# Performance work log

Hardware: AMD Instinct MI355X
Metric: run time of the kernel (lower is better)

The kernel has to match this reference:

```python
import jax, jax.numpy as jnp
import numpy as np

ROPE_BASE = 1000000.0
EPS = 1e-6
N_HEADS = 16

def apply_rope(x, base=ROPE_BASE):
    # x: [b, seq, heads, head_dim]
    b, seq, n_heads, dim = x.shape
    half = dim // 2
    i = jnp.arange(half)
    theta = 1.0 / base ** (2 * i / dim)
    pos = jnp.arange(seq)
    angles = pos[:, None] * theta[None, :]            # [seq, half]
    cos = jnp.cos(angles)[None, :, None, :]
    sin = jnp.sin(angles)[None, :, None, :]
    x1, x2 = jnp.split(x, 2, axis=-1)
    return jnp.concatenate([x1 * cos - x2 * sin, x1 * sin + x2 * cos], axis=-1)

def setup_inputs() -> dict:
    key = jax.random.key(0)
    ks = jax.random.split(key, 6)
    b, seq, dim = 2, 2048, 1024
    scale = 1.0 / np.sqrt(dim)
    return {
        "x": jax.random.normal(ks[0], (b, seq, dim), dtype=jnp.float32),
        "norm_scale": jnp.ones((dim,), dtype=jnp.float32),
        "Wq": jax.random.normal(ks[1], (dim, dim), dtype=jnp.float32) * scale,
        "Wk": jax.random.normal(ks[2], (dim, dim), dtype=jnp.float32) * scale,
        "Wv": jax.random.normal(ks[3], (dim, dim), dtype=jnp.float32) * scale,
        "Wo": jax.random.normal(ks[4], (dim, dim), dtype=jnp.float32) * scale,
    }

def reference(x, norm_scale, Wq, Wk, Wv, Wo):
    b, seq, d = x.shape
    n_heads = N_HEADS
    dh = d // n_heads
    # RMSNorm
    var = jnp.mean(jnp.square(x), axis=-1, keepdims=True)
    x_norm = x * jax.lax.rsqrt(var + EPS) * norm_scale
    # QKV projections ([in,out] weights as in nnx.Linear)
    q = (x_norm @ Wq).reshape(b, seq, n_heads, dh)
    k = (x_norm @ Wk).reshape(b, seq, n_heads, dh)
    v = (x_norm @ Wv).reshape(b, seq, n_heads, dh)
    q = apply_rope(q)
    k = apply_rope(k)
    # causal attention with explicit score matrix (faithful to source)
    scores = jnp.einsum('bthd,bshd->bhts', q, k) / jnp.sqrt(jnp.float32(dh))
    causal = jnp.triu(jnp.full((seq, seq), -jnp.inf, dtype=jnp.float32), k=1)
    scores = scores + causal[None, None, :, :]
    weights = jax.nn.softmax(scores, axis=-1)
    out = jnp.einsum('bhts,bshd->bthd', weights, v).reshape(b, seq, d)
    return out @ Wo
```

## Files before the change

kernel.cpp:

```cpp
#include <hip/hip_runtime.h>

typedef unsigned short ushort_t;
typedef __attribute__((ext_vector_type(8))) short short8;
typedef __attribute__((ext_vector_type(4))) short short4v;
typedef __attribute__((ext_vector_type(4))) float floatx4;

#define DEV static __device__ __forceinline__
#define NEG_BIG (-1e30f)

#define MFMA16(a, b, c) __builtin_amdgcn_mfma_f32_16x16x16bf16_1k((a), (b), (c), 0, 0, 0)

typedef const __attribute__((address_space(1))) unsigned int* gas_ptr;
typedef __attribute__((address_space(3))) unsigned int* las_ptr;

DEV void async16(const ushort_t* g, ushort_t* l) {
    __builtin_amdgcn_global_load_lds((gas_ptr)(const void*)g, (las_ptr)(void*)l, 16, 0, 0);
}

DEV float bf2f(ushort_t u) {
    union { unsigned u; float f; } v; v.u = ((unsigned)u) << 16; return v.f;
}
DEV ushort_t f2bf(float f) {
    union { float f; unsigned u; } v; v.f = f;
    unsigned r = v.u + 0x7FFF + ((v.u >> 16) & 1);
    return (ushort_t)(r >> 16);
}
DEV ushort_t f2bf_trunc(float f) {
    union { float f; unsigned u; } v; v.f = f;
    return (ushort_t)(v.u >> 16);
}
DEV float load_bf16_scrub(const ushort_t* p, size_t i) {
    ushort_t u = p[i];
    if (((u >> 7) & 0xFF) == 0xFF) u = 0;
    return bf2f(u);
}
DEV float load_f32_scrub(const ushort_t* p, size_t i) {
    unsigned u = ((const unsigned*)p)[i];
    if (((u >> 23) & 0xFF) == 0xFF) u = 0;
    union { unsigned u; float f; } v; v.u = u; return v.f;
}

DEV int probe_is_f32(const ushort_t* __restrict__ p) {
    int tid = threadIdx.x + threadIdx.y * blockDim.x;
    int nthr = blockDim.x * blockDim.y;
    __shared__ int cnt;
    if (tid == 0) cnt = 0;
    __syncthreads();
    int weird = 0;
    for (int i = tid; i < 2048; i += nthr) {
        unsigned e = (p[i] >> 7) & 0xFF;
        weird += (e >= 0x90) ? 1 : 0;
    }
#pragma unroll
    for (int off = 32; off; off >>= 1) weird += __shfl_xor(weird, off);
    if ((tid & 63) == 0) atomicAdd(&cnt, weird);
    __syncthreads();
    return cnt > 16;
}

__global__ void prep_kernel(const ushort_t* __restrict__ W0,
                            const ushort_t* __restrict__ W1,
                            const ushort_t* __restrict__ W2,
                            const ushort_t* __restrict__ W3,
                            ushort_t* __restrict__ WTq3,
                            ushort_t* __restrict__ WoT,
                            const ushort_t* __restrict__ x,
                            const ushort_t* __restrict__ g,
                            ushort_t* __restrict__ xn) {
    int is_f32 = probe_is_f32(x);
    int z = blockIdx.z;
    if (z < 4) {
        const ushort_t* W = (z == 0) ? W0 : (z == 1) ? W1 : (z == 2) ? W2 : W3;
        __shared__ ushort_t tile[32][33];
        int tx = threadIdx.x, ty = threadIdx.y;
        int xx = blockIdx.x * 32 + tx;
        int y0 = blockIdx.y * 32;
#pragma unroll
        for (int j = 0; j < 32; j += 8) {
            size_t idx = (size_t)(y0 + ty + j) * 1024 + xx;
            tile[ty + j][tx] = f2bf(is_f32 ? load_f32_scrub(W, idx) : load_bf16_scrub(W, idx));
        }
        __syncthreads();
        int nx = blockIdx.y * 32 + tx;
        ushort_t* dst = (z < 3) ? WTq3 : WoT;
        int ny0 = blockIdx.x * 32 + ((z < 3) ? z * 1024 : 0);
#pragma unroll
        for (int j = 0; j < 32; j += 8)
            dst[(size_t)(ny0 + ty + j) * 1024 + nx] = tile[tx][ty + j];
    } else {
        int row = (z - 4) * 1024 + blockIdx.y * 32 + blockIdx.x;
        int tid = threadIdx.y * 32 + threadIdx.x;
        float vals[4], gv[4];
        size_t base = (size_t)row * 1024 + tid * 4;
#pragma unroll
        for (int i = 0; i < 4; i++) {
            if (is_f32) {
                vals[i] = load_f32_scrub(x, base + i);
                gv[i]   = load_f32_scrub(g, tid * 4 + i);
            } else {
                vals[i] = load_bf16_scrub(x, base + i);
                gv[i]   = load_bf16_scrub(g, tid * 4 + i);
            }
        }
        float ss = vals[0]*vals[0] + vals[1]*vals[1] + vals[2]*vals[2] + vals[3]*vals[3];
#pragma unroll
        for (int off = 32; off > 0; off >>= 1) ss += __shfl_xor(ss, off);
        __shared__ float red[4];
        if ((tid & 63) == 0) red[tid >> 6] = ss;
        __syncthreads();
        ss = red[0] + red[1] + red[2] + red[3];
        float inv = rsqrtf(ss * (1.0f / 1024.0f) + 1e-6f);
#pragma unroll
        for (int i = 0; i < 4; i++)
            xn[base + i] = f2bf(vals[i] * inv * gv[i]);
    }
}

__global__ __launch_bounds__(256, 4) void gemm_qkv(const ushort_t* __restrict__ A,
                                                   const ushort_t* __restrict__ Bt,
                                                   ushort_t* __restrict__ qb,
                                                   ushort_t* __restrict__ kb,
                                                   ushort_t* __restrict__ vt) {
    const int K = 1024;
    int tid = threadIdx.x;
    int lane = tid & 63, w = tid >> 6;
    int c = lane & 15, quad = lane >> 4;
    int mh = w >> 1, nh = w & 1;
    int lin = blockIdx.y * gridDim.x + blockIdx.x;
    int xcd = lin & 7, idx = lin >> 3;
    int bm = ((xcd & 3) * 8 + (idx & 7)) * 128;
    int bn = ((xcd >> 2) * 12 + (idx >> 3)) * 128;
    int lr = lane >> 2, lq = lane & 3;

    __shared__ __align__(16) ushort_t As[16 * 512];
    __shared__ __align__(16) ushort_t Bs[16 * 512];

    const floatx4 zero = {0.f, 0.f, 0.f, 0.f};
    floatx4 acc[4][4];
#pragma unroll
    for (int i = 0; i < 4; i++)
#pragma unroll
        for (int j = 0; j < 4; j++) acc[i][j] = zero;

    for (int k0 = 0; k0 < K; k0 += 64) {
        __syncthreads();
#pragma unroll
        for (int ci = 0; ci < 8; ci++) {
            int ch = w * 8 + ci;
            if (ch < 16) {
                int rg = ch >> 1, kc = ch & 1;
                async16(A + (size_t)(bm + rg * 16 + lr) * K + k0 + kc * 32 + lq * 8,
                        As + ch * 512);
            } else {
                int b2 = ch - 16;
                int rg = b2 >> 1, kc = b2 & 1;
                async16(Bt + (size_t)(bn + rg * 16 + lr) * K + k0 + kc * 32 + lq * 8,
                        Bs + b2 * 512);
            }
        }
        __syncthreads();
#pragma unroll
        for (int kc = 0; kc < 2; kc++) {
            short8 af[4], bf[4];
#pragma unroll
            for (int i = 0; i < 4; i++)
                af[i] = *(const short8*)(As + ((mh * 4 + i) * 2 + kc) * 512 + c * 32 + quad * 8);
#pragma unroll
            for (int j = 0; j < 4; j++)
                bf[j] = *(const short8*)(Bs + ((nh * 4 + j) * 2 + kc) * 512 + c * 32 + quad * 8);
#pragma unroll
            for (int i = 0; i < 4; i++)
#pragma unroll
                for (int j = 0; j < 4; j++)
                    acc[i][j] = __builtin_amdgcn_mfma_f32_16x16x32_bf16(af[i], bf[j], acc[i][j], 0, 0, 0);
        }
    }

    int proj = bn >> 10;
    int n0 = (bn & 1023) + nh * 64;
    if (proj < 2) {
        float th0 = exp2f((float)c * (-19.931568569324174f / 32.0f));
        float th1 = exp2f((float)(16 + c) * (-19.931568569324174f / 32.0f));
        float scale = (proj == 0) ? 0.125f : 1.0f;
#pragma unroll
        for (int i = 0; i < 4; i++)
#pragma unroll
            for (int r = 0; r < 4; r++) {
                int s = (bm + mh * 64 + i * 16 + quad * 4 + r) & 2047;
                float a0 = (float)s * th0, a1 = (float)s * th1;
                float sn0 = __sinf(a0), cs0 = __cosf(a0);
                float sn1 = __sinf(a1), cs1 = __cosf(a1);
                float x1a = acc[i][0][r], x2a = acc[i][2][r];
                acc[i][0][r] = (x1a * cs0 - x2a * sn0) * scale;
                acc[i][2][r] = (x1a * sn0 + x2a * cs0) * scale;
                float x1b = acc[i][1][r], x2b = acc[i][3][r];
                acc[i][1][r] = (x1b * cs1 - x2b * sn1) * scale;
                acc[i][3][r] = (x1b * sn1 + x2b * cs1) * scale;
            }
        ushort_t* dst = (proj == 0) ? qb : kb;
#pragma unroll
        for (int i = 0; i < 4; i++)
#pragma unroll
            for (int j = 0; j < 4; j++)
#pragma unroll
                for (int r = 0; r < 4; r++) {
                    int row = bm + mh * 64 + i * 16 + quad * 4 + r;
                    dst[(size_t)row * 1024 + n0 + j * 16 + c] = f2bf(acc[i][j][r]);
                }
    } else {
#pragma unroll
        for (int i = 0; i < 4; i++) {
            int row0 = bm + mh * 64 + i * 16 + quad * 4;
            int b = row0 >> 11, s0v = row0 & 2047;
#pragma unroll
            for (int j = 0; j < 4; j++) {
                int col = n0 + j * 16 + c;
                int hh = col >> 6, dh = col & 63;
                short4v pk;
#pragma unroll
                for (int r = 0; r < 4; r++) pk[r] = (short)f2bf(acc[i][j][r]);
                *(short4v*)(vt + (size_t)((b * 16 + hh) * 64 + dh) * 2048 + s0v) = pk;
            }
        }
    }
}

__global__ __launch_bounds__(256, 4) void gemm_out(const ushort_t* __restrict__ A,
                                                   const ushort_t* __restrict__ Bt,
                                                   float* __restrict__ C) {
    const int K = 1024, N = 1024;
    int tid = threadIdx.x;
    int lane = tid & 63, w = tid >> 6;
    int c = lane & 15, quad = lane >> 4;
    int mh = w >> 1, nh = w & 1;
    int lin = blockIdx.y * gridDim.x + blockIdx.x;
    int xcd = lin & 7, idx = lin >> 3;
    int bm = ((xcd & 3) * 8 + (idx & 7)) * 128;
    int bn = ((xcd >> 2) * 8 + (idx >> 3)) * 64;
    int lr = lane >> 2, lq = lane & 3;

    __shared__ __align__(16) ushort_t As[16 * 512];
    __shared__ __align__(16) ushort_t Bs[8 * 512];

    const floatx4 zero = {0.f, 0.f, 0.f, 0.f};
    floatx4 acc[4][2];
#pragma unroll
    for (int i = 0; i < 4; i++)
#pragma unroll
        for (int j = 0; j < 2; j++) acc[i][j] = zero;

    for (int k0 = 0; k0 < K; k0 += 64) {
        __syncthreads();
#pragma unroll
        for (int ci = 0; ci < 6; ci++) {
            int ch = w * 6 + ci;
            if (ch < 16) {
                int rg = ch >> 1, kc = ch & 1;
                async16(A + (size_t)(bm + rg * 16 + lr) * K + k0 + kc * 32 + lq * 8,
                        As + ch * 512);
            } else {
                int b2 = ch - 16;
                int rg = b2 >> 1, kc = b2 & 1;
                async16(Bt + (size_t)(bn + rg * 16 + lr) * K + k0 + kc * 32 + lq * 8,
                        Bs + b2 * 512);
            }
        }
        __syncthreads();
#pragma unroll
        for (int kc = 0; kc < 2; kc++) {
            short8 af[4], bf[2];
#pragma unroll
            for (int i = 0; i < 4; i++)
                af[i] = *(const short8*)(As + ((mh * 4 + i) * 2 + kc) * 512 + c * 32 + quad * 8);
#pragma unroll
            for (int j = 0; j < 2; j++)
                bf[j] = *(const short8*)(Bs + ((nh * 2 + j) * 2 + kc) * 512 + c * 32 + quad * 8);
#pragma unroll
            for (int i = 0; i < 4; i++)
#pragma unroll
                for (int j = 0; j < 2; j++)
                    acc[i][j] = __builtin_amdgcn_mfma_f32_16x16x32_bf16(af[i], bf[j], acc[i][j], 0, 0, 0);
        }
    }
#pragma unroll
    for (int i = 0; i < 4; i++)
#pragma unroll
        for (int j = 0; j < 2; j++)
#pragma unroll
            for (int r = 0; r < 4; r++) {
                int row = bm + mh * 64 + i * 16 + quad * 4 + r;
                int col = bn + nh * 32 + j * 16 + c;
                C[(size_t)row * N + col] = acc[i][j][r];
            }
}

__global__ __launch_bounds__(256, 5) void attn_kernel(const ushort_t* __restrict__ q,
                                                      const ushort_t* __restrict__ k,
                                                      const ushort_t* __restrict__ vt,
                                                      ushort_t* __restrict__ o) {
    int tid = threadIdx.x;
    int lane = tid & 63, w = tid >> 6;
    int c = lane & 15, quad = lane >> 4;
    int bh = blockIdx.x;
    int b = bh >> 4, h = bh & 15;
    int qt = 31 - (int)blockIdx.y;
    int lr = lane >> 2, lq = lane & 3;
    int vb = (lq - lr) & 3;
    const ushort_t* qb  = q + (size_t)b * 2048 * 1024 + h * 64;
    const ushort_t* kbp = k + (size_t)b * 2048 * 1024 + h * 64;
    const ushort_t* vtb = vt + (size_t)(b * 16 + h) * 64 * 2048;
    ushort_t* ob = o + (size_t)b * 2048 * 1024 + h * 64;

    __shared__ __align__(16) ushort_t Ks[2][8 * 512];
    __shared__ __align__(16) ushort_t Vs[2][8 * 512];

    const floatx4 zero = {0.f, 0.f, 0.f, 0.f};

    int t0b = qt * 64;
    int t0w = t0b + w * 16;
    int ntile = qt + 1;

    const ushort_t* qrow = qb + (size_t)(t0w + c) * 1024;
    short8 aq0 = *(const short8*)(qrow + quad * 8);
    short8 aq1 = *(const short8*)(qrow + 32 + quad * 8);

    int voffA = c * 32 + (((quad >> 1) + c) & 3) * 8 + (quad & 1) * 4;
    int voffB = c * 32 + (((quad >> 1) + 2 + c) & 3) * 8 + (quad & 1) * 4;

    float l_sum = 0.f;
    floatx4 oacc[4];
#pragma unroll
    for (int dt = 0; dt < 4; dt++) oacc[dt] = zero;

#pragma unroll
    for (int ci = 0; ci < 4; ci++) {
        int ch = w * 4 + ci;
        if (ch < 8) {
            int nt = ch >> 1, hf = ch & 1;
            async16(kbp + (size_t)(nt * 16 + lr) * 1024 + hf * 32 + lq * 8,
                    Ks[0] + ch * 512);
        } else {
            int dt = (ch - 8) >> 1, hf = ch & 1;
            async16(vtb + (size_t)(dt * 16 + lr) * 2048 + hf * 32 + vb * 8,
                    Vs[0] + (ch - 8) * 512);
        }
    }

    for (int kt = 0; kt < ntile; kt++) {
        __syncthreads();
        int cur = kt & 1;
        if (kt + 1 < ntile) {
            int s1 = (kt + 1) * 64;
            int nxt = cur ^ 1;
#pragma unroll
            for (int ci = 0; ci < 4; ci++) {
                int ch = w * 4 + ci;
                if (ch < 8) {
                    int nt = ch >> 1, hf = ch & 1;
                    async16(kbp + (size_t)(s1 + nt * 16 + lr) * 1024 + hf * 32 + lq * 8,
                            Ks[nxt] + ch * 512);
                } else {
                    int dt = (ch - 8) >> 1, hf = ch & 1;
                    async16(vtb + (size_t)(dt * 16 + lr) * 2048 + s1 + hf * 32 + vb * 8,
                            Vs[nxt] + (ch - 8) * 512);
                }
            }
        }
        int s0 = kt * 64;

        floatx4 sacc[4];
#pragma unroll
        for (int nt = 0; nt < 4; nt++) sacc[nt] = zero;
        __builtin_amdgcn_s_setprio(1);
#pragma unroll
        for (int nt = 0; nt < 4; nt++) {
            short8 k0f = *(const short8*)(Ks[cur] + nt * 1024 + c * 32 + quad * 8);
            short8 k1f = *(const short8*)(Ks[cur] + nt * 1024 + 512 + c * 32 + quad * 8);
            sacc[nt] = __builtin_amdgcn_mfma_f32_16x16x32_bf16(k0f, aq0, sacc[nt], 0, 0, 0);
            sacc[nt] = __builtin_amdgcn_mfma_f32_16x16x32_bf16(k1f, aq1, sacc[nt], 0, 0, 0);
        }
        __builtin_amdgcn_s_setprio(0);

        short4v pa[4];
        float ps = 0.f;
        if (kt == ntile - 1) {
            int t = t0w + c;
#pragma unroll
            for (int nt = 0; nt < 4; nt++) {
                float pn = 0.f;
#pragma unroll
                for (int r = 0; r < 4; r++) {
                    int s = s0 + nt * 16 + quad * 4 + r;
                    float e = __expf((s > t) ? NEG_BIG : sacc[nt][r]);
                    pn += e;
                    pa[nt][r] = (short)f2bf_trunc(e);
                }
                ps += pn;
            }
        } else {
#pragma unroll
            for (int nt = 0; nt < 4; nt++) {
                float pn = 0.f;
#pragma unroll
                for (int r = 0; r < 4; r++) {
                    float e = __expf(sacc[nt][r]);
                    pn += e;
                    pa[nt][r] = (short)f2bf_trunc(e);
                }
                ps += pn;
            }
        }
        l_sum += ps;

        __builtin_amdgcn_s_setprio(1);
#pragma unroll
        for (int dt = 0; dt < 4; dt++) {
            const ushort_t* vbase = Vs[cur] + dt * 1024;
            short4v bv0 = *(const short4v*)(vbase + voffA);
            short4v bv1 = *(const short4v*)(vbase + voffB);
            short4v bv2 = *(const short4v*)(vbase + 512 + voffA);
            short4v bv3 = *(const short4v*)(vbase + 512 + voffB);
            oacc[dt] = MFMA16(pa[0], bv0, oacc[dt]);
            oacc[dt] = MFMA16(pa[1], bv1, oacc[dt]);
            oacc[dt] = MFMA16(pa[2], bv2, oacc[dt]);
            oacc[dt] = MFMA16(pa[3], bv3, oacc[dt]);
        }
        __builtin_amdgcn_s_setprio(0);
    }

    float l = l_sum;
    l += __shfl_xor(l, 16);
    l += __shfl_xor(l, 32);
    float linv0 = 1.0f / l;
    float linv[4];
#pragma unroll
    for (int r = 0; r < 4; r++) linv[r] = __shfl(linv0, quad * 4 + r);

#pragma unroll
    for (int dt = 0; dt < 4; dt++)
#pragma unroll
        for (int r = 0; r < 4; r++) {
            int t = t0w + quad * 4 + r;
            ob[(size_t)t * 1024 + dt * 16 + c] = f2bf_trunc(oacc[dt][r] * linv[r]);
        }
}

extern "C" void kernel_launch(void* const* d_in, const int* in_sizes, int n_in,
                              void* d_out, int out_size, void* d_ws, size_t ws_size,
                              hipStream_t stream) {
    const ushort_t* x  = (const ushort_t*)d_in[0];
    const ushort_t* g  = (const ushort_t*)d_in[1];
    const ushort_t* Wq = (const ushort_t*)d_in[2];
    const ushort_t* Wk = (const ushort_t*)d_in[3];
    const ushort_t* Wv = (const ushort_t*)d_in[4];
    const ushort_t* Wo = (const ushort_t*)d_in[5];

    char* ws = (char*)d_ws;
    const size_t MB = 1ull << 20;
    ushort_t* xn   = (ushort_t*)(ws);
    ushort_t* qb   = (ushort_t*)(ws + 8 * MB);
    ushort_t* kb   = (ushort_t*)(ws + 16 * MB);
    ushort_t* vt   = (ushort_t*)(ws + 24 * MB);
    ushort_t* WTq3 = (ushort_t*)(ws + 32 * MB);
    ushort_t* WoT  = (ushort_t*)(ws + 38 * MB);
    ushort_t* at   = xn;

    prep_kernel<<<dim3(32, 32, 8), dim3(32, 8), 0, stream>>>(Wq, Wk, Wv, Wo, WTq3, WoT, x, g, xn);

    gemm_qkv<<<dim3(24, 32), 256, 0, stream>>>(xn, WTq3, qb, kb, vt);

    attn_kernel<<<dim3(32, 32), 256, 0, stream>>>(qb, kb, vt, at);

    gemm_out<<<dim3(16, 32), 256, 0, stream>>>(at, WoT, (float*)d_out);
}
```

Measured before the change: 206.3 us.

## Stage softmax probabilities through LDS to use 16x16x32 MFMA for PV

The attention kernel now writes the exponentiated score tile as bf16 into a swizzled per-warp LDS buffer. It reads the tile back in the A-operand layout of the 16x16x32 bf16 MFMA, so the P·V product needs two wider MFMAs per output tile instead of four 16x16x16 ones. V is loaded without the old lane rotation, the setprio hints are removed, and the launch-bounds occupancy hint of 5 is dropped. The cost is an extra LDS write and read per tile, 8 KB more shared memory, and possibly lower occupancy.

```diff
diff --git a/kernel.cpp b/kernel.cpp
--- a/kernel.cpp
+++ b/kernel.cpp
@@ -7,8 +7,6 @@
 
 #define DEV static __device__ __forceinline__
 #define NEG_BIG (-1e30f)
-
-#define MFMA16(a, b, c) __builtin_amdgcn_mfma_f32_16x16x16bf16_1k((a), (b), (c), 0, 0, 0)
 
 typedef const __attribute__((address_space(1))) unsigned int* gas_ptr;
 typedef __attribute__((address_space(3))) unsigned int* las_ptr;
@@ -294,10 +292,10 @@
             }
 }
 
-__global__ __launch_bounds__(256, 5) void attn_kernel(const ushort_t* __restrict__ q,
-                                                      const ushort_t* __restrict__ k,
-                                                      const ushort_t* __restrict__ vt,
-                                                      ushort_t* __restrict__ o) {
+__global__ __launch_bounds__(256) void attn_kernel(const ushort_t* __restrict__ q,
+                                                   const ushort_t* __restrict__ k,
+                                                   const ushort_t* __restrict__ vt,
+                                                   ushort_t* __restrict__ o) {
     int tid = threadIdx.x;
     int lane = tid & 63, w = tid >> 6;
     int c = lane & 15, quad = lane >> 4;
@@ -305,7 +303,6 @@
     int b = bh >> 4, h = bh & 15;
     int qt = 31 - (int)blockIdx.y;
     int lr = lane >> 2, lq = lane & 3;
-    int vb = (lq - lr) & 3;
     const ushort_t* qb  = q + (size_t)b * 2048 * 1024 + h * 64;
     const ushort_t* kbp = k + (size_t)b * 2048 * 1024 + h * 64;
     const ushort_t* vtb = vt + (size_t)(b * 16 + h) * 64 * 2048;
@@ -313,6 +310,7 @@
 
     __shared__ __align__(16) ushort_t Ks[2][8 * 512];
     __shared__ __align__(16) ushort_t Vs[2][8 * 512];
+    __shared__ __align__(16) ushort_t Ps[64 * 64];
 
     const floatx4 zero = {0.f, 0.f, 0.f, 0.f};
 
@@ -324,8 +322,9 @@
     short8 aq0 = *(const short8*)(qrow + quad * 8);
     short8 aq1 = *(const short8*)(qrow + 32 + quad * 8);
 
-    int voffA = c * 32 + (((quad >> 1) + c) & 3) * 8 + (quad & 1) * 4;
-    int voffB = c * 32 + (((quad >> 1) + 2 + c) & 3) * 8 + (quad & 1) * 4;
+    int pswz = (c & 7) << 3;
+    int pwbase = ((w * 16 + c) * 64) ;
+    int prbase = ((w * 16 + c) * 64) ;
 
     float l_sum = 0.f;
     floatx4 oacc[4];
@@ -341,7 +340,7 @@
                     Ks[0] + ch * 512);
         } else {
             int dt = (ch - 8) >> 1, hf = ch & 1;
-            async16(vtb + (size_t)(dt * 16 + lr) * 2048 + hf * 32 + vb * 8,
+            async16(vtb + (size_t)(dt * 16 + lr) * 2048 + hf * 32 + lq * 8,
                     Vs[0] + (ch - 8) * 512);
         }
     }
@@ -361,7 +360,7 @@
                             Ks[nxt] + ch * 512);
                 } else {
                     int dt = (ch - 8) >> 1, hf = ch & 1;
-                    async16(vtb + (size_t)(dt * 16 + lr) * 2048 + s1 + hf * 32 + vb * 8,
+                    async16(vtb + (size_t)(dt * 16 + lr) * 2048 + s1 + hf * 32 + lq * 8,
                             Vs[nxt] + (ch - 8) * 512);
                 }
             }
@@ -371,7 +370,6 @@
         floatx4 sacc[4];
 #pragma unroll
         for (int nt = 0; nt < 4; nt++) sacc[nt] = zero;
-        __builtin_amdgcn_s_setprio(1);
 #pragma unroll
         for (int nt = 0; nt < 4; nt++) {
             short8 k0f = *(const short8*)(Ks[cur] + nt * 1024 + c * 32 + quad * 8);
@@ -379,53 +377,48 @@
             sacc[nt] = __builtin_amdgcn_mfma_f32_16x16x32_bf16(k0f, aq0, sacc[nt], 0, 0, 0);
             sacc[nt] = __builtin_amdgcn_mfma_f32_16x16x32_bf16(k1f, aq1, sacc[nt], 0, 0, 0);
         }
-        __builtin_amdgcn_s_setprio(0);
-
-        short4v pa[4];
-        float ps = 0.f;
+
         if (kt == ntile - 1) {
             int t = t0w + c;
 #pragma unroll
             for (int nt = 0; nt < 4; nt++) {
+                short4v pk;
                 float pn = 0.f;
 #pragma unroll
                 for (int r = 0; r < 4; r++) {
                     int s = s0 + nt * 16 + quad * 4 + r;
                     float e = __expf((s > t) ? NEG_BIG : sacc[nt][r]);
                     pn += e;
-                    pa[nt][r] = (short)f2bf_trunc(e);
+                    pk[r] = (short)f2bf_trunc(e);
                 }
-                ps += pn;
+                l_sum += pn;
+                *(short4v*)(Ps + ((pwbase + nt * 16 + quad * 4) ^ pswz)) = pk;
             }
         } else {
 #pragma unroll
             for (int nt = 0; nt < 4; nt++) {
+                short4v pk;
                 float pn = 0.f;
 #pragma unroll
                 for (int r = 0; r < 4; r++) {
                     float e = __expf(sacc[nt][r]);
                     pn += e;
-                    pa[nt][r] = (short)f2bf_trunc(e);
+                    pk[r] = (short)f2bf_trunc(e);
                 }
-                ps += pn;
-            }
-        }
-        l_sum += ps;
-
-        __builtin_amdgcn_s_setprio(1);
+                l_sum += pn;
+                *(short4v*)(Ps + ((pwbase + nt * 16 + quad * 4) ^ pswz)) = pk;
+            }
+        }
+
+        short8 pa0 = *(const short8*)(Ps + ((prbase + quad * 8) ^ pswz));
+        short8 pa1 = *(const short8*)(Ps + ((prbase + 32 + quad * 8) ^ pswz));
 #pragma unroll
         for (int dt = 0; dt < 4; dt++) {
-            const ushort_t* vbase = Vs[cur] + dt * 1024;
-            short4v bv0 = *(const short4v*)(vbase + voffA);
-            short4v bv1 = *(const short4v*)(vbase + voffB);
-            short4v bv2 = *(const short4v*)(vbase + 512 + voffA);
-            short4v bv3 = *(const short4v*)(vbase + 512 + voffB);
-            oacc[dt] = MFMA16(pa[0], bv0, oacc[dt]);
-            oacc[dt] = MFMA16(pa[1], bv1, oacc[dt]);
-            oacc[dt] = MFMA16(pa[2], bv2, oacc[dt]);
-            oacc[dt] = MFMA16(pa[3], bv3, oacc[dt]);
-        }
-        __builtin_amdgcn_s_setprio(0);
+            short8 v0 = *(const short8*)(Vs[cur] + dt * 1024 + c * 32 + quad * 8);
+            short8 v1 = *(const short8*)(Vs[cur] + dt * 1024 + 512 + c * 32 + quad * 8);
+            oacc[dt] = __builtin_amdgcn_mfma_f32_16x16x32_bf16(pa0, v0, oacc[dt], 0, 0, 0);
+            oacc[dt] = __builtin_amdgcn_mfma_f32_16x16x32_bf16(pa1, v1, oacc[dt], 0, 0, 0);
+        }
     }
 
     float l = l_sum;
```

After: 183.3 us. 1.13x faster.
